# Kernel optimization log

Hardware: AMD Instinct MI355X
Metric: run time of the kernel (lower is better)

Reference implementation:

```python
import jax, jax.numpy as jnp
import numpy as np

D_IN, D, K, N_CLASSES = 384, 512, 6, 2
SCALE = D ** (-0.5)

def _linear_params(key, fan_in, fan_out):
    kw, kb = jax.random.split(key)
    w = jax.random.normal(kw, (fan_in, fan_out), jnp.float32) * 0.02
    b = jax.random.normal(kb, (fan_out,), jnp.float32) * 0.01
    return w, b

def setup_inputs() -> dict:
    key = jax.random.key(0)
    ks = jax.random.split(key, 10)
    x = jax.random.normal(ks[0], (16384, D_IN), jnp.float32)
    fc1_w, fc1_b = _linear_params(ks[1], D_IN, D)
    wh_w, wh_b = _linear_params(ks[2], D, D)
    wt_w, wt_b = _linear_params(ks[3], D, D)
    lin1_w, lin1_b = _linear_params(ks[4], D, D)
    lin2_w, lin2_b = _linear_params(ks[5], D, D)
    att1_w, att1_b = _linear_params(ks[6], D, D // 2)
    att2_w, att2_b = _linear_params(ks[7], D // 2, 1)
    ln_g = jnp.ones((D,), jnp.float32)
    ln_b = jnp.zeros((D,), jnp.float32)
    fc_w, fc_b = _linear_params(ks[8], D, N_CLASSES)
    return dict(x=x, fc1_w=fc1_w, fc1_b=fc1_b, wh_w=wh_w, wh_b=wh_b,
                wt_w=wt_w, wt_b=wt_b, lin1_w=lin1_w, lin1_b=lin1_b,
                lin2_w=lin2_w, lin2_b=lin2_b, att1_w=att1_w, att1_b=att1_b,
                att2_w=att2_w, att2_b=att2_b, ln_g=ln_g, ln_b=ln_b,
                fc_w=fc_w, fc_b=fc_b)

def _forward(x, fc1_w, fc1_b, wh_w, wh_b, wt_w, wt_b, lin1_w, lin1_b,
             lin2_w, lin2_b, att1_w, att1_b, att2_w, att2_b, ln_g, ln_b,
             fc_w, fc_b):
    lrelu = jax.nn.leaky_relu  # slope 0.01, matches nn.LeakyReLU default
    h = lrelu(x @ fc1_w + fc1_b)                    # [N, D]
    h = (h + h.mean(axis=0, keepdims=True)) * 0.5
    e_h = h @ wh_w + wh_b                           # [N, D]
    e_t = h @ wt_w + wt_b                           # [N, D]
    attn_logit = (e_h * SCALE) @ e_t.T              # [N, N]
    topk_w, topk_i = jax.lax.top_k(attn_logit, K)   # [N, K]
    Nb = e_t[topk_i]                                # gather neighbors [N, K, D]
    p = jax.nn.softmax(topk_w, axis=-1)             # [N, K]
    eh_r = p[..., None] * Nb + (1.0 - p)[..., None] * e_h[:, None, :]
    gate = jnp.tanh(e_h[:, None, :] + eh_r)         # [N, K, D]
    # faithful to torch.einsum('ijkl,ijkm->ijk', Nb, gate): product of sums
    ka_w = Nb.sum(axis=-1) * gate.sum(axis=-1)      # [N, K]
    ka_p = jax.nn.softmax(ka_w, axis=-1)
    e_Nh = jnp.einsum('nk,nkd->nd', ka_p, Nb)       # [N, D]
    sum_emb = lrelu((e_h + e_Nh) @ lin1_w + lin1_b)
    bi_emb = lrelu((e_h * e_Nh) @ lin2_w + lin2_b)
    emb = sum_emb + bi_emb                          # [N, D] (dropout=eval, identity)
    # GlobalAttention readout
    a = lrelu(emb @ att1_w + att1_b) @ att2_w + att2_b  # [N, 1]
    g = jax.nn.softmax(a, axis=0)
    pooled = (g * emb).sum(axis=0, keepdims=True)   # [1, D]
    mu = pooled.mean(axis=-1, keepdims=True)
    var = pooled.var(axis=-1, keepdims=True)
    normed = (pooled - mu) * jax.lax.rsqrt(var + 1e-5) * ln_g + ln_b
    logits = normed @ fc_w + fc_b                   # [1, n_classes]
    return logits

def reference(x, fc1_w, fc1_b, wh_w, wh_b, wt_w, wt_b, lin1_w, lin1_b,
              lin2_w, lin2_b, att1_w, att1_b, att2_w, att2_b, ln_g, ln_b,
              fc_w, fc_b):
    logits = _forward(x, fc1_w, fc1_b, wh_w, wh_b, wt_w, wt_b, lin1_w, lin1_b,
                      lin2_w, lin2_b, att1_w, att1_b, att2_w, att2_b,
                      ln_g, ln_b, fc_w, fc_b)
    y_prob = jax.nn.softmax(logits, axis=-1)
    return logits, y_prob
```

## Files before the change

kernel.cpp:

```cpp
#include <hip/hip_runtime.h>
#include <math.h>

#define NROWS 16384
#define DIN   384
#define DIM   512
#define KSEL  6
#define NSPLIT 4
#define COLS_PER_SPLIT (NROWS / NSPLIT)
#define ATT_SCALE 0.044194173824159216f

typedef unsigned short u16;
typedef __attribute__((ext_vector_type(8))) short bf16x8;
typedef __attribute__((ext_vector_type(16))) float f32x16;

static __device__ __forceinline__ float lrelu_f(float v) {
  return v > 0.f ? v : 0.01f * v;
}

static __device__ __forceinline__ u16 f2bf(float f) {
  unsigned u = __float_as_uint(f);
  unsigned r = (u + 0x7FFFu + ((u >> 16) & 1u)) >> 16;
  return (u16)r;
}

static __device__ __forceinline__ void sbar() {
  asm volatile("" ::: "memory");
  __builtin_amdgcn_s_barrier();
  asm volatile("" ::: "memory");
}

__global__ __launch_bounds__(256)
void convx(const float* __restrict__ X, u16* __restrict__ Xb) {
  int i = blockIdx.x * 256 + threadIdx.x;
  const float4* p = (const float4*)X + (size_t)i * 2;
  float4 a = p[0], b = p[1];
  uint4 o;
  o.x = f2bf(a.x) | ((unsigned)f2bf(a.y) << 16);
  o.y = f2bf(a.z) | ((unsigned)f2bf(a.w) << 16);
  o.z = f2bf(b.x) | ((unsigned)f2bf(b.y) << 16);
  o.w = f2bf(b.z) | ((unsigned)f2bf(b.w) << 16);
  ((uint4*)Xb)[i] = o;
}

__global__ __launch_bounds__(256)
void wconv(const float* __restrict__ W, u16* __restrict__ Wt, int K, int N) {
  int t = blockIdx.x * 256 + threadIdx.x;
  if (t >= K * N) return;
  int k = t / N, n = t - k * N;
  Wt[(size_t)n * K + k] = f2bf(W[t]);
}

__global__ __launch_bounds__(256)
void colsum_partial(const float* __restrict__ H, float* __restrict__ part) {
  int col = blockIdx.x * 64 + (threadIdx.x & 63);
  int sub = threadIdx.x >> 6;
  int rEnd = blockIdx.y * 512 + 512;
  float s = 0.f;
  for (int r = blockIdx.y * 512 + sub; r < rEnd; r += 4)
    s += H[(size_t)r * DIM + col];
  __shared__ float sh[4][64];
  sh[sub][threadIdx.x & 63] = s;
  __syncthreads();
  if (threadIdx.x < 64) {
    float tot = sh[0][threadIdx.x] + sh[1][threadIdx.x] +
                sh[2][threadIdx.x] + sh[3][threadIdx.x];
    part[(size_t)blockIdx.y * DIM + col] = tot;
  }
}

__global__ void finalize_mean(const float* __restrict__ part,
                              float* __restrict__ mean) {
  int c = threadIdx.x;
  float s = 0.f;
  for (int j = 0; j < 32; j++) s += part[j * DIM + c];
  mean[c] = s * (1.0f / NROWS);
}

__global__ __launch_bounds__(256)
void h_fix_bf(const float* __restrict__ H0, const float* __restrict__ mean,
              u16* __restrict__ Hb) {
  int idx = blockIdx.x * 256 + threadIdx.x;
  int c = (idx * 8) & (DIM - 1);
  const float4* p = (const float4*)H0 + (size_t)idx * 2;
  float4 a = p[0], b = p[1];
  float4 m0 = *(const float4*)(mean + c);
  float4 m1 = *(const float4*)(mean + c + 4);
  a.x = (a.x + m0.x) * 0.5f; a.y = (a.y + m0.y) * 0.5f;
  a.z = (a.z + m0.z) * 0.5f; a.w = (a.w + m0.w) * 0.5f;
  b.x = (b.x + m1.x) * 0.5f; b.y = (b.y + m1.y) * 0.5f;
  b.z = (b.z + m1.z) * 0.5f; b.w = (b.w + m1.w) * 0.5f;
  uint4 o;
  o.x = f2bf(a.x) | ((unsigned)f2bf(a.y) << 16);
  o.y = f2bf(a.z) | ((unsigned)f2bf(a.w) << 16);
  o.z = f2bf(b.x) | ((unsigned)f2bf(b.y) << 16);
  o.w = f2bf(b.z) | ((unsigned)f2bf(b.w) << 16);
  ((uint4*)Hb)[idx] = o;
}

template<int ACT, int ACCUM, int STOREBF>
__global__ __launch_bounds__(256, 2)
void gemm_bf16(const u16* __restrict__ A, const u16* __restrict__ Wt,
               const float* __restrict__ bias, float* __restrict__ C,
               u16* __restrict__ Cb, float bscale, int K, int N) {
  __shared__ char lds[65536];
  const int tid = threadIdx.x;
  const int w = tid >> 6, l = tid & 63;
  const int l31 = l & 31, lh = l >> 5, lh16 = lh << 4;
  const int qg = w & 1, ng = w >> 1;
  const int swz = (l31 & 7) << 4;
  const int rowBase = blockIdx.y * 128;
  const int colBase = blockIdx.x * 128;
  const int nsteps = K >> 6;

  f32x16 z;
  #pragma unroll
  for (int i = 0; i < 16; i++) z[i] = 0.f;
  f32x16 acc00 = z, acc01 = z, acc10 = z, acc11 = z;

#define GSTAGE(buf_, kc_) do { \
    const int r_ = tid >> 3, j_ = tid & 7; \
    const int js_ = ((j_ ^ (r_ & 7)) << 3); \
    const u16* as_ = A + (size_t)rowBase * K + (kc_); \
    const u16* ws_ = Wt + (size_t)colBase * K + (kc_); \
    char* ab_ = lds + (buf_) * 16384; \
    char* wb_ = lds + 32768 + (buf_) * 16384; \
    _Pragma("unroll") \
    for (int p_ = 0; p_ < 4; ++p_) { \
      __builtin_amdgcn_global_load_lds( \
        (const __attribute__((address_space(1))) void*)(as_ + (size_t)(r_ + 32 * p_) * K + js_), \
        (__attribute__((address_space(3))) void*)(ab_ + w * 1024 + p_ * 4096), 16, 0, 0); \
      __builtin_amdgcn_global_load_lds( \
        (const __attribute__((address_space(1))) void*)(ws_ + (size_t)(r_ + 32 * p_) * K + js_), \
        (__attribute__((address_space(3))) void*)(wb_ + w * 1024 + p_ * 4096), 16, 0, 0); \
    } \
  } while (0)

  GSTAGE(0, 0);
  asm volatile("s_waitcnt vmcnt(0)" ::: "memory");
  sbar();
  #pragma unroll 1
  for (int s = 0; s < nsteps; ++s) {
    const int cur = s & 1;
    if (s + 1 < nsteps) GSTAGE(cur ^ 1, (s + 1) * 64);
    __builtin_amdgcn_sched_barrier(0);
    const char* ab = lds + cur * 16384;
    const char* wb = lds + 32768 + cur * 16384;
    __builtin_amdgcn_s_setprio(1);
    #pragma unroll
    for (int s4 = 0; s4 < 4; ++s4) {
      const int off = (s4 * 32 + lh16) ^ swz;
      bf16x8 am0 = *(const bf16x8*)(ab + (qg * 64 + l31) * 128 + off);
      bf16x8 am1 = *(const bf16x8*)(ab + (qg * 64 + 32 + l31) * 128 + off);
      bf16x8 wn0 = *(const bf16x8*)(wb + (ng * 64 + l31) * 128 + off);
      bf16x8 wn1 = *(const bf16x8*)(wb + (ng * 64 + 32 + l31) * 128 + off);
      acc00 = __builtin_amdgcn_mfma_f32_32x32x16_bf16(wn0, am0, acc00, 0, 0, 0);
      acc01 = __builtin_amdgcn_mfma_f32_32x32x16_bf16(wn1, am0, acc01, 0, 0, 0);
      acc10 = __builtin_amdgcn_mfma_f32_32x32x16_bf16(wn0, am1, acc10, 0, 0, 0);
      acc11 = __builtin_amdgcn_mfma_f32_32x32x16_bf16(wn1, am1, acc11, 0, 0, 0);
    }
    __builtin_amdgcn_s_setprio(0);
    asm volatile("s_waitcnt vmcnt(0)" ::: "memory");
    sbar();
  }
#undef GSTAGE

  float* Ls = (float*)lds;
  {
    const int m0 = qg * 64 + l31;
    const int k0 = (m0 & 7) << 2;
    #pragma unroll
    for (int r = 0; r < 16; ++r) {
      const int nd = ng * 64 + (r & 3) + 8 * (r >> 2) + 4 * lh;
      Ls[m0 * 128 + (nd ^ k0)] = acc00[r];
      Ls[m0 * 128 + ((nd + 32) ^ k0)] = acc01[r];
      Ls[(m0 + 32) * 128 + (nd ^ k0)] = acc10[r];
      Ls[(m0 + 32) * 128 + ((nd + 32) ^ k0)] = acc11[r];
    }
  }
  sbar();
  #pragma unroll
  for (int p = 0; p < 16; ++p) {
    int idx = tid + 256 * p;
    int m = idx >> 5, c4 = (idx & 31) << 2;
    float4 v = *(const float4*)&Ls[m * 128 + (c4 ^ ((m & 7) << 2))];
    int col = colBase + c4;
    float4 bv = *(const float4*)&bias[col];
    v.x += bv.x; v.y += bv.y; v.z += bv.z; v.w += bv.w;
    if (ACT) {
      v.x = lrelu_f(v.x); v.y = lrelu_f(v.y);
      v.z = lrelu_f(v.z); v.w = lrelu_f(v.w);
    }
    size_t o = (size_t)(rowBase + m) * N + col;
    if (ACCUM) {
      float4 c0 = *(const float4*)&C[o];
      v.x += c0.x; v.y += c0.y; v.z += c0.z; v.w += c0.w;
    }
    *(float4*)&C[o] = v;
    if (STOREBF) {
      ushort4 q;
      q.x = f2bf(v.x * bscale); q.y = f2bf(v.y * bscale);
      q.z = f2bf(v.z * bscale); q.w = f2bf(v.w * bscale);
      *(ushort4*)&Cb[o] = q;
    }
  }
}

#define T6(tv, tix, vv, cc) do { float v_ = (vv); \
  if (v_ > tv[5]) { tv[5] = v_; tix[5] = (cc); \
    if (tv[5] > tv[4]) { float t=tv[4];tv[4]=tv[5];tv[5]=t; int q=tix[4];tix[4]=tix[5];tix[5]=q; } \
    if (tv[4] > tv[3]) { float t=tv[3];tv[3]=tv[4];tv[4]=t; int q=tix[3];tix[3]=tix[4];tix[4]=q; } \
    if (tv[3] > tv[2]) { float t=tv[2];tv[2]=tv[3];tv[3]=t; int q=tix[2];tix[2]=tix[3];tix[3]=q; } \
    if (tv[2] > tv[1]) { float t=tv[1];tv[1]=tv[2];tv[2]=t; int q=tix[1];tix[1]=tix[2];tix[2]=q; } \
    if (tv[1] > tv[0]) { float t=tv[0];tv[0]=tv[1];tv[1]=t; int q=tix[0];tix[0]=tix[1];tix[1]=q; } \
  } } while (0)

__global__ __launch_bounds__(256, 2)
void attn_topk_mfma(const u16* __restrict__ EHb, const u16* __restrict__ ETb,
                    float* __restrict__ TWp, int* __restrict__ TIp) {
  __shared__ char lds[65536];
  const int tid = threadIdx.x;
  const int w = tid >> 6, l = tid & 63;
  const int l31 = l & 31, lh = l >> 5, lh16 = lh << 4;
  const int qg = w & 1, ng = w >> 1;
  const int swz = (l31 & 7) << 4;

  const int bid = blockIdx.x;
  const int xcd = bid & 7;
  const int local = bid >> 3;
  const int split = local & 3;
  const int rowBase = (xcd * 16 + (local >> 2)) * 128;

  f32x16 z;
  #pragma unroll
  for (int i = 0; i < 16; i++) z[i] = 0.f;
  f32x16 acc00 = z, acc01 = z, acc10 = z, acc11 = z;

  float tvA[KSEL], tvB[KSEL]; int tixA[KSEL], tixB[KSEL];
  #pragma unroll
  for (int k = 0; k < KSEL; k++) {
    tvA[k] = -INFINITY; tixA[k] = 0; tvB[k] = -INFINITY; tixB[k] = 0;
  }

#define STAGE_AB(buf_, nct_, nkc_) do { \
    const int r_ = tid >> 3, j_ = tid & 7; \
    const int js_ = ((j_ ^ (r_ & 7)) << 3); \
    const u16* as_ = EHb + (size_t)rowBase * DIM + (nkc_) * 64; \
    const u16* bs_ = ETb + (size_t)(split * COLS_PER_SPLIT + (nct_) * 128) * DIM + (nkc_) * 64; \
    char* ab_ = lds + (buf_) * 16384; \
    char* bb_ = lds + 32768 + (buf_) * 16384; \
    _Pragma("unroll") \
    for (int p_ = 0; p_ < 4; ++p_) { \
      __builtin_amdgcn_global_load_lds( \
        (const __attribute__((address_space(1))) void*)(as_ + (size_t)(r_ + 32 * p_) * DIM + js_), \
        (__attribute__((address_space(3))) void*)(ab_ + w * 1024 + p_ * 4096), 16, 0, 0); \
      __builtin_amdgcn_global_load_lds( \
        (const __attribute__((address_space(1))) void*)(bs_ + (size_t)(r_ + 32 * p_) * DIM + js_), \
        (__attribute__((address_space(3))) void*)(bb_ + w * 1024 + p_ * 4096), 16, 0, 0); \
    } \
  } while (0)

  STAGE_AB(0, 0, 0);
  asm volatile("s_waitcnt vmcnt(0)" ::: "memory");
  sbar();
  #pragma unroll 1
  for (int s = 0; s < 256; ++s) {
    const int cur = s & 1;
    if (s + 1 < 256) {
      const int ns = s + 1;
      STAGE_AB(cur ^ 1, ns >> 3, ns & 7);
    }
    __builtin_amdgcn_sched_barrier(0);
    const char* ab = lds + cur * 16384;
    const char* bb = lds + 32768 + cur * 16384;
    __builtin_amdgcn_s_setprio(1);
    #pragma unroll
    for (int s4 = 0; s4 < 4; ++s4) {
      const int off = (s4 * 32 + lh16) ^ swz;
      bf16x8 aq0 = *(const bf16x8*)(ab + (qg * 64 + l31) * 128 + off);
      bf16x8 aq1 = *(const bf16x8*)(ab + (qg * 64 + 32 + l31) * 128 + off);
      bf16x8 bn0 = *(const bf16x8*)(bb + (ng * 64 + l31) * 128 + off);
      bf16x8 bn1 = *(const bf16x8*)(bb + (ng * 64 + 32 + l31) * 128 + off);
      acc00 = __builtin_amdgcn_mfma_f32_32x32x16_bf16(bn0, aq0, acc00, 0, 0, 0);
      acc01 = __builtin_amdgcn_mfma_f32_32x32x16_bf16(bn1, aq0, acc01, 0, 0, 0);
      acc10 = __builtin_amdgcn_mfma_f32_32x32x16_bf16(bn0, aq1, acc10, 0, 0, 0);
      acc11 = __builtin_amdgcn_mfma_f32_32x32x16_bf16(bn1, aq1, acc11, 0, 0, 0);
    }
    __builtin_amdgcn_s_setprio(0);
    if ((s & 7) == 7) {
      const int cb = split * COLS_PER_SPLIT + (s >> 3) * 128 + ng * 64 + 4 * lh;
      #pragma unroll
      for (int r = 0; r < 16; ++r) {
        const int nd = cb + (r & 3) + 8 * (r >> 2);
        T6(tvA, tixA, acc00[r], nd);
        T6(tvB, tixB, acc10[r], nd);
      }
      #pragma unroll
      for (int r = 0; r < 16; ++r) {
        const int nd = cb + 32 + (r & 3) + 8 * (r >> 2);
        T6(tvA, tixA, acc01[r], nd);
        T6(tvB, tixB, acc11[r], nd);
      }
      acc00 = z; acc01 = z; acc10 = z; acc11 = z;
    }
    asm volatile("s_waitcnt vmcnt(0)" ::: "memory");
    sbar();
  }
#undef STAGE_AB

  float* MV = (float*)lds;
  int* MI = (int*)(lds + 12288);
  {
    const int src = ng * 2 + lh;
    const int q0 = qg * 64 + l31;
    #pragma unroll
    for (int k = 0; k < KSEL; k++) {
      MV[(q0 * 4 + src) * 6 + k] = tvA[k];
      MI[(q0 * 4 + src) * 6 + k] = tixA[k];
      MV[((q0 + 32) * 4 + src) * 6 + k] = tvB[k];
      MI[((q0 + 32) * 4 + src) * 6 + k] = tixB[k];
    }
  }
  sbar();
  if (tid < 128) {
    int mb = tid * 24;
    unsigned used = 0;
    float ov[KSEL]; int oi[KSEL];
    #pragma unroll
    for (int s = 0; s < KSEL; ++s) {
      float bvv = -INFINITY; int bi = 0x7fffffff; int be = 0;
      for (int e = 0; e < 24; ++e) {
        if (used & (1u << e)) continue;
        float v = MV[mb + e]; int ix = MI[mb + e];
        if (v > bvv || (v == bvv && ix < bi)) { bvv = v; bi = ix; be = e; }
      }
      used |= 1u << be;
      ov[s] = bvv; oi[s] = bi;
    }
    size_t o = ((size_t)split * NROWS + rowBase + tid) * KSEL;
    #pragma unroll
    for (int k = 0; k < KSEL; k++) { TWp[o + k] = ov[k]; TIp[o + k] = oi[k]; }
  }
}

__global__ __launch_bounds__(256)
void topk_merge(const float* __restrict__ TWp, const int* __restrict__ TIp,
                float* __restrict__ TW, int* __restrict__ TI) {
  int row = blockIdx.x * 256 + threadIdx.x;
  float tv[KSEL]; int tix[KSEL];
  #pragma unroll
  for (int k = 0; k < KSEL; k++) { tv[k] = -INFINITY; tix[k] = 0x7fffffff; }
  #pragma unroll
  for (int s = 0; s < NSPLIT; s++) {
    size_t o = ((size_t)s * NROWS + row) * KSEL;
    #pragma unroll
    for (int k = 0; k < KSEL; k++) {
      float cv = TWp[o + k]; int ci = TIp[o + k];
      bool better5 = (cv > tv[5]) || (cv == tv[5] && ci < tix[5]);
      if (better5) {
        tv[5] = cv; tix[5] = ci;
        if ((tv[5] > tv[4]) || (tv[5] == tv[4] && tix[5] < tix[4])) {
          float t = tv[4]; tv[4] = tv[5]; tv[5] = t;
          int ti = tix[4]; tix[4] = tix[5]; tix[5] = ti; }
        if ((tv[4] > tv[3]) || (tv[4] == tv[3] && tix[4] < tix[3])) {
          float t = tv[3]; tv[3] = tv[4]; tv[4] = t;
          int ti = tix[3]; tix[3] = tix[4]; tix[4] = ti; }
        if ((tv[3] > tv[2]) || (tv[3] == tv[2] && tix[3] < tix[2])) {
          float t = tv[2]; tv[2] = tv[3]; tv[3] = t;
          int ti = tix[2]; tix[2] = tix[3]; tix[3] = ti; }
        if ((tv[2] > tv[1]) || (tv[2] == tv[1] && tix[2] < tix[1])) {
          float t = tv[1]; tv[1] = tv[2]; tv[2] = t;
          int ti = tix[1]; tix[1] = tix[2]; tix[2] = ti; }
        if ((tv[1] > tv[0]) || (tv[1] == tv[0] && tix[1] < tix[0])) {
          float t = tv[0]; tv[0] = tv[1]; tv[1] = t;
          int ti = tix[0]; tix[0] = tix[1]; tix[1] = ti; }
      }
    }
  }
  size_t o = (size_t)row * KSEL;
  #pragma unroll
  for (int k = 0; k < KSEL; k++) { TW[o + k] = tv[k]; TI[o + k] = tix[k]; }
}

__global__ __launch_bounds__(256)
void neighbor_kernel(const float* __restrict__ EH, const float* __restrict__ ET,
                     const float* __restrict__ TW, const int* __restrict__ TI,
                     u16* __restrict__ SINb, u16* __restrict__ BINb) {
  const int lane = threadIdx.x & 63;
  const int row = blockIdx.x * 4 + (threadIdx.x >> 6);
  const float* eh = EH + (size_t)row * DIM;
  float ehv[8];
  #pragma unroll
  for (int u = 0; u < 8; u++) ehv[u] = eh[u * 64 + lane];
  float tw[KSEL]; int ti[KSEL];
  #pragma unroll
  for (int k = 0; k < KSEL; k++) {
    tw[k] = TW[(size_t)row * KSEL + k];
    ti[k] = TI[(size_t)row * KSEL + k];
  }
  float m = tw[0];
  #pragma unroll
  for (int k = 1; k < KSEL; k++) m = fmaxf(m, tw[k]);
  float p[KSEL], ps = 0.f;
  #pragma unroll
  for (int k = 0; k < KSEL; k++) { p[k] = expf(tw[k] - m); ps += p[k]; }
  float inv = 1.f / ps;
  #pragma unroll
  for (int k = 0; k < KSEL; k++) p[k] *= inv;

  float nb[KSEL][8];
  float kaw[KSEL];
  #pragma unroll
  for (int k = 0; k < KSEL; k++) {
    const float* et = ET + (size_t)ti[k] * DIM;
    float snb = 0.f, sg = 0.f;
    #pragma unroll
    for (int u = 0; u < 8; u++) {
      float nbv = et[u * 64 + lane];
      nb[k][u] = nbv;
      float ehr = p[k] * nbv + (1.f - p[k]) * ehv[u];
      float g = tanhf(ehv[u] + ehr);
      snb += nbv; sg += g;
    }
    #pragma unroll
    for (int off = 32; off > 0; off >>= 1) {
      snb += __shfl_xor(snb, off);
      sg  += __shfl_xor(sg, off);
    }
    kaw[k] = snb * sg;
  }
  float km = kaw[0];
  #pragma unroll
  for (int k = 1; k < KSEL; k++) km = fmaxf(km, kaw[k]);
  float kp[KSEL], ks = 0.f;
  #pragma unroll
  for (int k = 0; k < KSEL; k++) { kp[k] = expf(kaw[k] - km); ks += kp[k]; }
  float kinv = 1.f / ks;
  #pragma unroll
  for (int k = 0; k < KSEL; k++) kp[k] *= kinv;

  #pragma unroll
  for (int u = 0; u < 8; u++) {
    float enh = 0.f;
    #pragma unroll
    for (int k = 0; k < KSEL; k++) enh += kp[k] * nb[k][u];
    size_t o = (size_t)row * DIM + u * 64 + lane;
    SINb[o] = f2bf(ehv[u] + enh);
    BINb[o] = f2bf(ehv[u] * enh);
  }
}

__global__ __launch_bounds__(256)
void att2_kernel(const float* __restrict__ HID, const float* __restrict__ w2,
                 const float* __restrict__ b2, float* __restrict__ ASC) {
  const int lane = threadIdx.x & 63;
  const int row = blockIdx.x * 4 + (threadIdx.x >> 6);
  float4 hv = ((const float4*)(HID + (size_t)row * 256))[lane];
  float4 wv = ((const float4*)w2)[lane];
  float s = hv.x * wv.x + hv.y * wv.y + hv.z * wv.z + hv.w * wv.w;
  #pragma unroll
  for (int off = 32; off > 0; off >>= 1) s += __shfl_xor(s, off);
  if (lane == 0) ASC[row] = s + b2[0];
}

__global__ __launch_bounds__(1024)
void areduce(const float* __restrict__ ASC, float* __restrict__ stats) {
  __shared__ float sm[1024];
  int t = threadIdx.x;
  float m = -INFINITY;
  for (int i = t; i < NROWS; i += 1024) m = fmaxf(m, ASC[i]);
  sm[t] = m; __syncthreads();
  for (int s = 512; s > 0; s >>= 1) {
    if (t < s) sm[t] = fmaxf(sm[t], sm[t + s]);
    __syncthreads();
  }
  float mx = sm[0]; __syncthreads();
  float sum = 0.f;
  for (int i = t; i < NROWS; i += 1024) sum += expf(ASC[i] - mx);
  sm[t] = sum; __syncthreads();
  for (int s = 512; s > 0; s >>= 1) {
    if (t < s) sm[t] += sm[t + s];
    __syncthreads();
  }
  if (t == 0) { stats[0] = mx; stats[1] = sm[0]; }
}

__global__ __launch_bounds__(256)
void pooled_partial(const float* __restrict__ EMB, const float* __restrict__ ASC,
                    const float* __restrict__ stats, float* __restrict__ part) {
  int col = blockIdx.x * 64 + (threadIdx.x & 63);
  int sub = threadIdx.x >> 6;
  float mx = stats[0];
  int rEnd = blockIdx.y * 512 + 512;
  float s = 0.f;
  for (int r = blockIdx.y * 512 + sub; r < rEnd; r += 4)
    s += expf(ASC[r] - mx) * EMB[(size_t)r * DIM + col];
  __shared__ float sh[4][64];
  sh[sub][threadIdx.x & 63] = s;
  __syncthreads();
  if (threadIdx.x < 64) {
    float tot = sh[0][threadIdx.x] + sh[1][threadIdx.x] +
                sh[2][threadIdx.x] + sh[3][threadIdx.x];
    part[(size_t)blockIdx.y * DIM + col] = tot;
  }
}

__global__ __launch_bounds__(512)
void final_kernel(const float* __restrict__ part, const float* __restrict__ stats,
                  const float* __restrict__ ln_g, const float* __restrict__ ln_b,
                  const float* __restrict__ fc_w, const float* __restrict__ fc_b,
                  float* __restrict__ out) {
  __shared__ float sh[512];
  int t = threadIdx.x;
  float s = 0.f;
  for (int j = 0; j < 32; j++) s += part[j * DIM + t];
  float pooled = s / stats[1];
  sh[t] = pooled; __syncthreads();
  for (int off = 256; off > 0; off >>= 1) {
    if (t < off) sh[t] += sh[t + off];
    __syncthreads();
  }
  float mu = sh[0] * (1.f / DIM); __syncthreads();
  float dv = pooled - mu;
  sh[t] = dv * dv; __syncthreads();
  for (int off = 256; off > 0; off >>= 1) {
    if (t < off) sh[t] += sh[t + off];
    __syncthreads();
  }
  float var = sh[0] * (1.f / DIM); __syncthreads();
  float normed = dv * rsqrtf(var + 1e-5f) * ln_g[t] + ln_b[t];
  sh[t] = normed * fc_w[t * 2 + 0]; __syncthreads();
  for (int off = 256; off > 0; off >>= 1) {
    if (t < off) sh[t] += sh[t + off];
    __syncthreads();
  }
  float l0 = sh[0] + fc_b[0]; __syncthreads();
  sh[t] = normed * fc_w[t * 2 + 1]; __syncthreads();
  for (int off = 256; off > 0; off >>= 1) {
    if (t < off) sh[t] += sh[t + off];
    __syncthreads();
  }
  float l1 = sh[0] + fc_b[1];
  if (t == 0) {
    float mm = fmaxf(l0, l1);
    float e0 = expf(l0 - mm), e1 = expf(l1 - mm);
    float si = 1.f / (e0 + e1);
    out[0] = l0; out[1] = l1; out[2] = e0 * si; out[3] = e1 * si;
  }
}

extern "C" void kernel_launch(void* const* d_in, const int* in_sizes, int n_in,
                              void* d_out, int out_size, void* d_ws, size_t ws_size,
                              hipStream_t stream) {
  (void)in_sizes; (void)n_in; (void)out_size; (void)ws_size;
  const float* x      = (const float*)d_in[0];
  const float* fc1_w  = (const float*)d_in[1];
  const float* fc1_b  = (const float*)d_in[2];
  const float* wh_w   = (const float*)d_in[3];
  const float* wh_b   = (const float*)d_in[4];
  const float* wt_w   = (const float*)d_in[5];
  const float* wt_b   = (const float*)d_in[6];
  const float* lin1_w = (const float*)d_in[7];
  const float* lin1_b = (const float*)d_in[8];
  const float* lin2_w = (const float*)d_in[9];
  const float* lin2_b = (const float*)d_in[10];
  const float* att1_w = (const float*)d_in[11];
  const float* att1_b = (const float*)d_in[12];
  const float* att2_w = (const float*)d_in[13];
  const float* att2_b = (const float*)d_in[14];
  const float* ln_g   = (const float*)d_in[15];
  const float* ln_b   = (const float*)d_in[16];
  const float* fc_w   = (const float*)d_in[17];
  const float* fc_b   = (const float*)d_in[18];
  float* out = (float*)d_out;

  char* ws = (char*)d_ws;
  float* B0   = (float*)(ws);
  float* B1   = (float*)(ws + 33554432);
  float* B2   = (float*)(ws + 67108864);
  float* TWp  = (float*)(ws + 100663296);
  int*   TIp  = (int*)  (ws + 100663296 + 1572864);
  float* TW   = (float*)(ws + 100663296 + 3145728);
  int*   TI   = (int*)  (ws + 100663296 + 3145728 + 393216);
  float* part = (float*)(ws + 100663296 + 3145728 + 786432);
  float* mean = (float*)(ws + 100663296 + 3145728 + 786432 + 65536);
  float* ascr = (float*)(ws + 100663296 + 3145728 + 786432 + 65536 + 2048);
  float* stats= (float*)(ws + 100663296 + 3145728 + 786432 + 65536 + 2048 + 65536);
  u16*   hb   = (u16*)(ws + 104732672);
  u16*   EHb  = (u16*)(ws + 104732672 + 16777216);
  u16*   ETb  = (u16*)(ws + 104732672 + 33554432);
  u16*   WT   = (u16*)(ws + 104732672 + 50331648);
  u16* fc1t = WT;
  u16* wht  = fc1t + 196608;
  u16* wtt  = wht + 262144;
  u16* lin1t= wtt + 262144;
  u16* lin2t= lin1t + 262144;
  u16* att1t= lin2t + 262144;
  u16* xb   = (u16*)B1;
  u16* sinb = EHb;
  u16* binb = ETb;
  u16* embb = hb;

  convx<<<3072, 256, 0, stream>>>(x, xb);
  wconv<<<768, 256, 0, stream>>>(fc1_w, fc1t, 384, 512);
  wconv<<<1024, 256, 0, stream>>>(wh_w, wht, 512, 512);
  wconv<<<1024, 256, 0, stream>>>(wt_w, wtt, 512, 512);
  wconv<<<1024, 256, 0, stream>>>(lin1_w, lin1t, 512, 512);
  wconv<<<1024, 256, 0, stream>>>(lin2_w, lin2t, 512, 512);
  wconv<<<512, 256, 0, stream>>>(att1_w, att1t, 512, 256);
  gemm_bf16<1,0,0><<<dim3(4,128), 256, 0, stream>>>(xb, fc1t, fc1_b, B0, nullptr, 1.f, 384, 512);
  colsum_partial<<<dim3(8,32), 256, 0, stream>>>(B0, part);
  finalize_mean<<<1, 512, 0, stream>>>(part, mean);
  h_fix_bf<<<4096, 256, 0, stream>>>(B0, mean, hb);
  gemm_bf16<0,0,1><<<dim3(4,128), 256, 0, stream>>>(hb, wht, wh_b, B1, EHb, ATT_SCALE, 512, 512);
  gemm_bf16<0,0,1><<<dim3(4,128), 256, 0, stream>>>(hb, wtt, wt_b, B2, ETb, 1.f, 512, 512);
  attn_topk_mfma<<<512, 256, 0, stream>>>(EHb, ETb, TWp, TIp);
  topk_merge<<<64, 256, 0, stream>>>(TWp, TIp, TW, TI);
  neighbor_kernel<<<4096, 256, 0, stream>>>(B1, B2, TW, TI, sinb, binb);
  gemm_bf16<1,0,0><<<dim3(4,128), 256, 0, stream>>>(sinb, lin1t, lin1_b, B2, nullptr, 1.f, 512, 512);
  gemm_bf16<1,1,1><<<dim3(4,128), 256, 0, stream>>>(binb, lin2t, lin2_b, B2, embb, 1.f, 512, 512);
  gemm_bf16<1,0,0><<<dim3(2,128), 256, 0, stream>>>(embb, att1t, att1_b, B0, nullptr, 1.f, 512, 256);
  att2_kernel<<<4096, 256, 0, stream>>>(B0, att2_w, att2_b, ascr);
  areduce<<<1, 1024, 0, stream>>>(ascr, stats);
  pooled_partial<<<dim3(8,32), 256, 0, stream>>>(B2, ascr, stats, part);
  final_kernel<<<1, 512, 0, stream>>>(part, stats, ln_g, ln_b, fc_w, fc_b, out);
}
```

Before: 681.6 us.

## Widen attention top-k tile to 256 columns with 512 threads and triple buffering

The attention+top-k kernel now runs 512 threads per block. Each step processes a 128x256 tile instead of 128x128, and the LDS ring grows from double to triple buffering (144KB), with prefetch two stages ahead and a partial vmcnt wait. This halves the number of barrier-separated steps and keeps more loads in flight to hide global latency. The cost is occupancy of one block per CU and a larger final merge (48 candidates per row instead of 24).

Result: slower. 852.6 us (+25.1%).

```diff
diff --git a/kernel.cpp b/kernel.cpp
--- a/kernel.cpp
+++ b/kernel.cpp
@@ -214,10 +214,10 @@
     if (tv[1] > tv[0]) { float t=tv[0];tv[0]=tv[1];tv[1]=t; int q=tix[0];tix[0]=tix[1];tix[1]=q; } \
   } } while (0)
 
-__global__ __launch_bounds__(256, 2)
+__global__ __launch_bounds__(512, 1)
 void attn_topk_mfma(const u16* __restrict__ EHb, const u16* __restrict__ ETb,
                     float* __restrict__ TWp, int* __restrict__ TIp) {
-  __shared__ char lds[65536];
+  __shared__ char lds[147456];
   const int tid = threadIdx.x;
   const int w = tid >> 6, l = tid & 63;
   const int l31 = l & 31, lh = l >> 5, lh16 = lh << 4;
@@ -241,37 +241,39 @@
     tvA[k] = -INFINITY; tixA[k] = 0; tvB[k] = -INFINITY; tixB[k] = 0;
   }
 
-#define STAGE_AB(buf_, nct_, nkc_) do { \
+#define STAGE(bufi_, ns_) do { \
+    const int ct_ = (ns_) >> 3, kc_ = (ns_) & 7; \
     const int r_ = tid >> 3, j_ = tid & 7; \
     const int js_ = ((j_ ^ (r_ & 7)) << 3); \
-    const u16* as_ = EHb + (size_t)rowBase * DIM + (nkc_) * 64; \
-    const u16* bs_ = ETb + (size_t)(split * COLS_PER_SPLIT + (nct_) * 128) * DIM + (nkc_) * 64; \
-    char* ab_ = lds + (buf_) * 16384; \
-    char* bb_ = lds + 32768 + (buf_) * 16384; \
+    const u16* as_ = EHb + (size_t)rowBase * DIM + kc_ * 64; \
+    const u16* bs_ = ETb + (size_t)(split * COLS_PER_SPLIT + ct_ * 256) * DIM + kc_ * 64; \
+    char* ab_ = lds + (bufi_) * 49152; \
+    char* bb_ = ab_ + 16384; \
+    _Pragma("unroll") \
+    for (int p_ = 0; p_ < 2; ++p_) { \
+      __builtin_amdgcn_global_load_lds( \
+        (const __attribute__((address_space(1))) void*)(as_ + (size_t)(r_ + 64 * p_) * DIM + js_), \
+        (__attribute__((address_space(3))) void*)(ab_ + (tid + 512 * p_) * 16), 16, 0, 0); \
+    } \
     _Pragma("unroll") \
     for (int p_ = 0; p_ < 4; ++p_) { \
       __builtin_amdgcn_global_load_lds( \
-        (const __attribute__((address_space(1))) void*)(as_ + (size_t)(r_ + 32 * p_) * DIM + js_), \
-        (__attribute__((address_space(3))) void*)(ab_ + w * 1024 + p_ * 4096), 16, 0, 0); \
-      __builtin_amdgcn_global_load_lds( \
-        (const __attribute__((address_space(1))) void*)(bs_ + (size_t)(r_ + 32 * p_) * DIM + js_), \
-        (__attribute__((address_space(3))) void*)(bb_ + w * 1024 + p_ * 4096), 16, 0, 0); \
+        (const __attribute__((address_space(1))) void*)(bs_ + (size_t)(r_ + 64 * p_) * DIM + js_), \
+        (__attribute__((address_space(3))) void*)(bb_ + (tid + 512 * p_) * 16), 16, 0, 0); \
     } \
   } while (0)
 
-  STAGE_AB(0, 0, 0);
-  asm volatile("s_waitcnt vmcnt(0)" ::: "memory");
+  int cur = 0, stg = 2;
+  STAGE(0, 0);
+  STAGE(1, 1);
+  asm volatile("s_waitcnt vmcnt(6)" ::: "memory");
   sbar();
   #pragma unroll 1
-  for (int s = 0; s < 256; ++s) {
-    const int cur = s & 1;
-    if (s + 1 < 256) {
-      const int ns = s + 1;
-      STAGE_AB(cur ^ 1, ns >> 3, ns & 7);
-    }
+  for (int s = 0; s < 128; ++s) {
+    if (s + 2 < 128) STAGE(stg, s + 2);
     __builtin_amdgcn_sched_barrier(0);
-    const char* ab = lds + cur * 16384;
-    const char* bb = lds + 32768 + cur * 16384;
+    const char* ab = lds + cur * 49152;
+    const char* bb = ab + 16384;
     __builtin_amdgcn_s_setprio(1);
     #pragma unroll
     for (int s4 = 0; s4 < 4; ++s4) {
@@ -287,7 +289,7 @@
     }
     __builtin_amdgcn_s_setprio(0);
     if ((s & 7) == 7) {
-      const int cb = split * COLS_PER_SPLIT + (s >> 3) * 128 + ng * 64 + 4 * lh;
+      const int cb = split * COLS_PER_SPLIT + (s >> 3) * 256 + ng * 64 + 4 * lh;
       #pragma unroll
       for (int r = 0; r < 16; ++r) {
         const int nd = cb + (r & 3) + 8 * (r >> 2);
@@ -302,38 +304,41 @@
       }
       acc00 = z; acc01 = z; acc10 = z; acc11 = z;
     }
-    asm volatile("s_waitcnt vmcnt(0)" ::: "memory");
+    if (s < 126) { asm volatile("s_waitcnt vmcnt(6)" ::: "memory"); }
+    else         { asm volatile("s_waitcnt vmcnt(0)" ::: "memory"); }
     sbar();
-  }
-#undef STAGE_AB
+    cur = (cur == 2) ? 0 : cur + 1;
+    stg = (stg == 2) ? 0 : stg + 1;
+  }
+#undef STAGE
 
   float* MV = (float*)lds;
-  int* MI = (int*)(lds + 12288);
+  int* MI = (int*)(lds + 24576);
   {
     const int src = ng * 2 + lh;
     const int q0 = qg * 64 + l31;
     #pragma unroll
     for (int k = 0; k < KSEL; k++) {
-      MV[(q0 * 4 + src) * 6 + k] = tvA[k];
-      MI[(q0 * 4 + src) * 6 + k] = tixA[k];
-      MV[((q0 + 32) * 4 + src) * 6 + k] = tvB[k];
-      MI[((q0 + 32) * 4 + src) * 6 + k] = tixB[k];
+      MV[(q0 * 8 + src) * 6 + k] = tvA[k];
+      MI[(q0 * 8 + src) * 6 + k] = tixA[k];
+      MV[((q0 + 32) * 8 + src) * 6 + k] = tvB[k];
+      MI[((q0 + 32) * 8 + src) * 6 + k] = tixB[k];
     }
   }
   sbar();
   if (tid < 128) {
-    int mb = tid * 24;
-    unsigned used = 0;
+    int mb = tid * 48;
+    unsigned long long used = 0ull;
     float ov[KSEL]; int oi[KSEL];
     #pragma unroll
     for (int s = 0; s < KSEL; ++s) {
       float bvv = -INFINITY; int bi = 0x7fffffff; int be = 0;
-      for (int e = 0; e < 24; ++e) {
-        if (used & (1u << e)) continue;
+      for (int e = 0; e < 48; ++e) {
+        if (used & (1ull << e)) continue;
         float v = MV[mb + e]; int ix = MI[mb + e];
         if (v > bvv || (v == bvv && ix < bi)) { bvv = v; bi = ix; be = e; }
       }
-      used |= 1u << be;
+      used |= 1ull << be;
       ov[s] = bvv; oi[s] = bi;
     }
     size_t o = ((size_t)split * NROWS + rowBase + tid) * KSEL;
@@ -613,7 +618,7 @@
   h_fix_bf<<<4096, 256, 0, stream>>>(B0, mean, hb);
   gemm_bf16<0,0,1><<<dim3(4,128), 256, 0, stream>>>(hb, wht, wh_b, B1, EHb, ATT_SCALE, 512, 512);
   gemm_bf16<0,0,1><<<dim3(4,128), 256, 0, stream>>>(hb, wtt, wt_b, B2, ETb, 1.f, 512, 512);
-  attn_topk_mfma<<<512, 256, 0, stream>>>(EHb, ETb, TWp, TIp);
+  attn_topk_mfma<<<512, 512, 0, stream>>>(EHb, ETb, TWp, TIp);
   topk_merge<<<64, 256, 0, stream>>>(TWp, TIp, TW, TI);
   neighbor_kernel<<<4096, 256, 0, stream>>>(B1, B2, TW, TI, sinb, binb);
   gemm_bf16<1,0,0><<<dim3(4,128), 256, 0, stream>>>(sinb, lin1t, lin1_b, B2, nullptr, 1.f, 512, 512);
```

## Hold query rows in registers and give each wave its own key pipeline

Applied to the files above, without the earlier changes.

The attention top-k kernel now keeps each wave's 32 query rows in registers for the full 512-wide reduction, so only the key tiles are streamed. Each wave gets a private double-buffered LDS region and waits with partial vmcnt counts, which removes the block-wide barriers. The final merge becomes a lane-pair shuffle instead of an LDS reduction over four sources. In exchange, each block now covers 128 rows per split with 64 columns per tile, which changes arithmetic intensity per load, and the 32 bf16x8 registers per lane raise register pressure.

New measurement: 667.1 us. -2.1%, faster.

```diff
diff --git a/kernel.cpp b/kernel.cpp
--- a/kernel.cpp
+++ b/kernel.cpp
@@ -220,125 +220,123 @@
   __shared__ char lds[65536];
   const int tid = threadIdx.x;
   const int w = tid >> 6, l = tid & 63;
-  const int l31 = l & 31, lh = l >> 5, lh16 = lh << 4;
-  const int qg = w & 1, ng = w >> 1;
-  const int swz = (l31 & 7) << 4;
+  const int l31 = l & 31, lh = l >> 5;
 
   const int bid = blockIdx.x;
   const int xcd = bid & 7;
-  const int local = bid >> 3;
-  const int split = local & 3;
-  const int rowBase = (xcd * 16 + (local >> 2)) * 128;
+  const int split = xcd & 3;
+  const int rowBase = ((xcd >> 2) * 64 + (bid >> 3)) * 128;
+  const int qrow = rowBase + w * 32 + l31;
+
+  bf16x8 areg[32];
+  {
+    const u16* ap = EHb + (size_t)qrow * DIM + lh * 8;
+    #pragma unroll
+    for (int ks = 0; ks < 32; ++ks)
+      areg[ks] = *(const bf16x8*)(ap + ks * 16);
+  }
+
+  char* ldsw = lds + w * 16384;
 
   f32x16 z;
   #pragma unroll
   for (int i = 0; i < 16; i++) z[i] = 0.f;
-  f32x16 acc00 = z, acc01 = z, acc10 = z, acc11 = z;
-
-  float tvA[KSEL], tvB[KSEL]; int tixA[KSEL], tixB[KSEL];
-  #pragma unroll
-  for (int k = 0; k < KSEL; k++) {
-    tvA[k] = -INFINITY; tixA[k] = 0; tvB[k] = -INFINITY; tixB[k] = 0;
-  }
-
-#define STAGE_AB(buf_, nct_, nkc_) do { \
-    const int r_ = tid >> 3, j_ = tid & 7; \
-    const int js_ = ((j_ ^ (r_ & 7)) << 3); \
-    const u16* as_ = EHb + (size_t)rowBase * DIM + (nkc_) * 64; \
-    const u16* bs_ = ETb + (size_t)(split * COLS_PER_SPLIT + (nct_) * 128) * DIM + (nkc_) * 64; \
-    char* ab_ = lds + (buf_) * 16384; \
-    char* bb_ = lds + 32768 + (buf_) * 16384; \
+  f32x16 acc0 = z, acc1 = z;
+
+  float tv[KSEL]; int tix[KSEL];
+  #pragma unroll
+  for (int k = 0; k < KSEL; k++) { tv[k] = -INFINITY; tix[k] = 0x7fffffff; }
+
+#define STAGE(buf_, ct_, kc_) do { \
+    char* db_ = ldsw + (buf_) * 8192; \
+    const u16* bs_ = ETb + (size_t)(split * COLS_PER_SPLIT + (ct_) * 64) * DIM + (kc_) * 64; \
     _Pragma("unroll") \
-    for (int p_ = 0; p_ < 4; ++p_) { \
+    for (int p_ = 0; p_ < 8; ++p_) { \
+      const int rn_ = p_ * 8 + (l >> 3); \
+      const int js_ = ((l & 7) ^ (rn_ & 7)) * 8; \
       __builtin_amdgcn_global_load_lds( \
-        (const __attribute__((address_space(1))) void*)(as_ + (size_t)(r_ + 32 * p_) * DIM + js_), \
-        (__attribute__((address_space(3))) void*)(ab_ + w * 1024 + p_ * 4096), 16, 0, 0); \
-      __builtin_amdgcn_global_load_lds( \
-        (const __attribute__((address_space(1))) void*)(bs_ + (size_t)(r_ + 32 * p_) * DIM + js_), \
-        (__attribute__((address_space(3))) void*)(bb_ + w * 1024 + p_ * 4096), 16, 0, 0); \
+        (const __attribute__((address_space(1))) void*)(bs_ + (size_t)rn_ * DIM + js_), \
+        (__attribute__((address_space(3))) void*)(db_ + p_ * 1024), 16, 0, 0); \
     } \
   } while (0)
 
-  STAGE_AB(0, 0, 0);
-  asm volatile("s_waitcnt vmcnt(0)" ::: "memory");
-  sbar();
+  STAGE(0, 0, 0);
+  STAGE(1, 0, 1);
+  asm volatile("s_waitcnt vmcnt(8)" ::: "memory");
+
   #pragma unroll 1
-  for (int s = 0; s < 256; ++s) {
-    const int cur = s & 1;
-    if (s + 1 < 256) {
-      const int ns = s + 1;
-      STAGE_AB(cur ^ 1, ns >> 3, ns & 7);
-    }
-    __builtin_amdgcn_sched_barrier(0);
-    const char* ab = lds + cur * 16384;
-    const char* bb = lds + 32768 + cur * 16384;
-    __builtin_amdgcn_s_setprio(1);
-    #pragma unroll
-    for (int s4 = 0; s4 < 4; ++s4) {
-      const int off = (s4 * 32 + lh16) ^ swz;
-      bf16x8 aq0 = *(const bf16x8*)(ab + (qg * 64 + l31) * 128 + off);
-      bf16x8 aq1 = *(const bf16x8*)(ab + (qg * 64 + 32 + l31) * 128 + off);
-      bf16x8 bn0 = *(const bf16x8*)(bb + (ng * 64 + l31) * 128 + off);
-      bf16x8 bn1 = *(const bf16x8*)(bb + (ng * 64 + 32 + l31) * 128 + off);
-      acc00 = __builtin_amdgcn_mfma_f32_32x32x16_bf16(bn0, aq0, acc00, 0, 0, 0);
-      acc01 = __builtin_amdgcn_mfma_f32_32x32x16_bf16(bn1, aq0, acc01, 0, 0, 0);
-      acc10 = __builtin_amdgcn_mfma_f32_32x32x16_bf16(bn0, aq1, acc10, 0, 0, 0);
-      acc11 = __builtin_amdgcn_mfma_f32_32x32x16_bf16(bn1, aq1, acc11, 0, 0, 0);
-    }
-    __builtin_amdgcn_s_setprio(0);
-    if ((s & 7) == 7) {
-      const int cb = split * COLS_PER_SPLIT + (s >> 3) * 128 + ng * 64 + 4 * lh;
+  for (int ct = 0; ct < 64; ++ct) {
+    #pragma unroll
+    for (int kc = 0; kc < 8; ++kc) {
+      const char* db = ldsw + (kc & 1) * 8192;
+      __builtin_amdgcn_s_setprio(1);
+      #pragma unroll
+      for (int s4 = 0; s4 < 4; ++s4) {
+        const int c0 = ((s4 * 2 + lh) ^ (l31 & 7)) * 16;
+        bf16x8 bn0 = *(const bf16x8*)(db + l31 * 128 + c0);
+        const int r1 = 32 + l31;
+        const int c1 = ((s4 * 2 + lh) ^ (r1 & 7)) * 16;
+        bf16x8 bn1 = *(const bf16x8*)(db + r1 * 128 + c1);
+        acc0 = __builtin_amdgcn_mfma_f32_32x32x16_bf16(bn0, areg[kc * 4 + s4], acc0, 0, 0, 0);
+        acc1 = __builtin_amdgcn_mfma_f32_32x32x16_bf16(bn1, areg[kc * 4 + s4], acc1, 0, 0, 0);
+      }
+      __builtin_amdgcn_s_setprio(0);
+      __builtin_amdgcn_sched_barrier(0);
+      if (!(ct == 63 && kc >= 6)) {
+        const int nct = (kc < 6) ? ct : ct + 1;
+        const int nkc = (kc + 2) & 7;
+        STAGE(kc & 1, nct, nkc);
+      }
+      if (ct == 63 && kc >= 5) { asm volatile("s_waitcnt vmcnt(0)" ::: "memory"); }
+      else                     { asm volatile("s_waitcnt vmcnt(8)" ::: "memory"); }
+    }
+    {
+      const int cb = split * COLS_PER_SPLIT + ct * 64 + 4 * lh;
       #pragma unroll
       for (int r = 0; r < 16; ++r) {
         const int nd = cb + (r & 3) + 8 * (r >> 2);
-        T6(tvA, tixA, acc00[r], nd);
-        T6(tvB, tixB, acc10[r], nd);
+        T6(tv, tix, acc0[r], nd);
+        T6(tv, tix, acc1[r], nd + 32);
       }
-      #pragma unroll
-      for (int r = 0; r < 16; ++r) {
-        const int nd = cb + 32 + (r & 3) + 8 * (r >> 2);
-        T6(tvA, tixA, acc01[r], nd);
-        T6(tvB, tixB, acc11[r], nd);
+      acc0 = z; acc1 = z;
+    }
+  }
+#undef STAGE
+
+  {
+    float pv[KSEL]; int pi[KSEL];
+    #pragma unroll
+    for (int k = 0; k < KSEL; k++) {
+      pv[k] = __shfl_xor(tv[k], 32);
+      pi[k] = __shfl_xor(tix[k], 32);
+    }
+    #pragma unroll
+    for (int k = 0; k < KSEL; k++) {
+      float cv = pv[k]; int ci = pi[k];
+      if ((cv > tv[5]) || (cv == tv[5] && ci < tix[5])) {
+        tv[5] = cv; tix[5] = ci;
+        if ((tv[5] > tv[4]) || (tv[5] == tv[4] && tix[5] < tix[4])) {
+          float t = tv[4]; tv[4] = tv[5]; tv[5] = t;
+          int q = tix[4]; tix[4] = tix[5]; tix[5] = q; }
+        if ((tv[4] > tv[3]) || (tv[4] == tv[3] && tix[4] < tix[3])) {
+          float t = tv[3]; tv[3] = tv[4]; tv[4] = t;
+          int q = tix[3]; tix[3] = tix[4]; tix[4] = q; }
+        if ((tv[3] > tv[2]) || (tv[3] == tv[2] && tix[3] < tix[2])) {
+          float t = tv[2]; tv[2] = tv[3]; tv[3] = t;
+          int q = tix[2]; tix[2] = tix[3]; tix[3] = q; }
+        if ((tv[2] > tv[1]) || (tv[2] == tv[1] && tix[2] < tix[1])) {
+          float t = tv[1]; tv[1] = tv[2]; tv[2] = t;
+          int q = tix[1]; tix[1] = tix[2]; tix[2] = q; }
+        if ((tv[1] > tv[0]) || (tv[1] == tv[0] && tix[1] < tix[0])) {
+          float t = tv[0]; tv[0] = tv[1]; tv[1] = t;
+          int q = tix[0]; tix[0] = tix[1]; tix[1] = q; }
       }
-      acc00 = z; acc01 = z; acc10 = z; acc11 = z;
-    }
-    asm volatile("s_waitcnt vmcnt(0)" ::: "memory");
-    sbar();
-  }
-#undef STAGE_AB
-
-  float* MV = (float*)lds;
-  int* MI = (int*)(lds + 12288);
-  {
-    const int src = ng * 2 + lh;
-    const int q0 = qg * 64 + l31;
-    #pragma unroll
-    for (int k = 0; k < KSEL; k++) {
-      MV[(q0 * 4 + src) * 6 + k] = tvA[k];
-      MI[(q0 * 4 + src) * 6 + k] = tixA[k];
-      MV[((q0 + 32) * 4 + src) * 6 + k] = tvB[k];
-      MI[((q0 + 32) * 4 + src) * 6 + k] = tixB[k];
-    }
-  }
-  sbar();
-  if (tid < 128) {
-    int mb = tid * 24;
-    unsigned used = 0;
-    float ov[KSEL]; int oi[KSEL];
-    #pragma unroll
-    for (int s = 0; s < KSEL; ++s) {
-      float bvv = -INFINITY; int bi = 0x7fffffff; int be = 0;
-      for (int e = 0; e < 24; ++e) {
-        if (used & (1u << e)) continue;
-        float v = MV[mb + e]; int ix = MI[mb + e];
-        if (v > bvv || (v == bvv && ix < bi)) { bvv = v; bi = ix; be = e; }
-      }
-      used |= 1u << be;
-      ov[s] = bvv; oi[s] = bi;
-    }
-    size_t o = ((size_t)split * NROWS + rowBase + tid) * KSEL;
-    #pragma unroll
-    for (int k = 0; k < KSEL; k++) { TWp[o + k] = ov[k]; TIp[o + k] = oi[k]; }
+    }
+  }
+  if (lh == 0) {
+    size_t o = ((size_t)split * NROWS + qrow) * KSEL;
+    #pragma unroll
+    for (int k = 0; k < KSEL; k++) { TWp[o + k] = tv[k]; TIp[o + k] = tix[k]; }
   }
 }
 
```
